# Performance work log

Measured on AMD Instinct MI355X. Metric: run time of the kernel, lower is better.

## Reference

```python
import jax, jax.numpy as jnp
import numpy as np

D_MODEL = 1024
N_HEADS = 16
B, T = 2, 2048


def setup_inputs() -> dict:
    key = jax.random.key(0)
    kx, kqkv, ko = jax.random.split(key, 3)
    x = jax.random.normal(kx, (B, T, D_MODEL), dtype=jnp.float32)
    # flax Linear default init (lecun_normal ~ scaled); plain scaled normal is fine for a baseline
    Wqkv = jax.random.normal(kqkv, (D_MODEL, 3 * D_MODEL), dtype=jnp.float32) / np.sqrt(D_MODEL)
    Wo = jax.random.normal(ko, (D_MODEL, D_MODEL), dtype=jnp.float32) / np.sqrt(D_MODEL)
    return {"x": x, "Wqkv": Wqkv, "Wo": Wo}


def reference(x, Wqkv, Wo):
    Bx, Tx, C = x.shape
    H = N_HEADS
    Hd = C // H
    scale = C ** (-0.5)  # NOTE: module scales by d_model**-0.5, not head_dim**-0.5
    qkv = x @ Wqkv  # [B, T, 3C]
    q, k, v = jnp.split(qkv, 3, axis=-1)
    q = q.reshape(Bx, Tx, H, Hd).transpose(0, 2, 1, 3)  # [B,H,T,Hd]
    k = k.reshape(Bx, Tx, H, Hd).transpose(0, 2, 1, 3)
    v = v.reshape(Bx, Tx, H, Hd).transpose(0, 2, 1, 3)
    attn = jnp.einsum('bhid,bhjd->bhij', q, k) * scale  # [B,H,T,T]
    mask = jnp.tril(jnp.ones((Tx, Tx), dtype=jnp.bool_))
    attn = jnp.where(mask[None, None], attn, jnp.finfo(attn.dtype).min)
    attn = jax.nn.softmax(attn.astype(jnp.float32), axis=-1).astype(attn.dtype)
    out = jnp.einsum('bhij,bhjd->bhid', attn, v)  # [B,H,T,Hd]
    out = out.transpose(0, 2, 1, 3).reshape(Bx, Tx, C)
    return out @ Wo
```

## Files before the change

kernel.cpp:

```cpp
#include <hip/hip_runtime.h>
#include <cstdint>
#include <math.h>

#define D_MODEL 1024
#define N_HEADS 16
#define HEAD_DIM 64
#define BB 2
#define TT 2048
#define QSCALE 0.04508422002778011f
#define MSTATIC 12.0f

typedef float f32x4 __attribute__((ext_vector_type(4)));
typedef __bf16 bf16x8 __attribute__((ext_vector_type(8)));

__device__ inline ushort f2bf(float f) {
    union { float f; uint32_t u; } c; c.f = f;
    uint32_t u = c.u;
    uint32_t r = (u + 0x7FFFu + ((u >> 16) & 1u)) >> 16;
    return (ushort)r;
}
__device__ inline ushort f2bf_hw(float f) {
    __bf16 h = (__bf16)f;
    return __builtin_bit_cast(ushort, h);
}

__device__ inline void load_lds16(const ushort* g, ushort* lds_uniform_base) {
    __builtin_amdgcn_global_load_lds(
        (const __attribute__((address_space(1))) uint32_t*)g,
        (__attribute__((address_space(3))) uint32_t*)lds_uniform_base, 16, 0, 0);
}

__global__ __launch_bounds__(256) void prep(
    const float4* __restrict__ xin, ushort4* __restrict__ xb,
    const float* __restrict__ Wqkv, ushort* __restrict__ WqkvT,
    const float* __restrict__ Wo, ushort* __restrict__ WoT)
{
    int bid = blockIdx.x;
    int tid = threadIdx.x;
    if (bid < 4096) {
        int i = bid * 256 + tid;
        float4 v = xin[i];
        ushort4 u;
        u.x = f2bf(v.x); u.y = f2bf(v.y); u.z = f2bf(v.z); u.w = f2bf(v.w);
        xb[i] = u;
        return;
    }
    __shared__ ushort tile[32][33];
    int tx = tid & 31, ty = tid >> 5;
    const float* in; ushort* out; int R, C, c0, r0;
    if (bid < 7168) {
        int b2 = bid - 4096;
        in = Wqkv; out = WqkvT; R = D_MODEL; C = 3 * D_MODEL;
        c0 = (b2 % 96) * 32; r0 = (b2 / 96) * 32;
    } else {
        int b3 = bid - 7168;
        in = Wo; out = WoT; R = D_MODEL; C = D_MODEL;
        c0 = (b3 % 32) * 32; r0 = (b3 / 32) * 32;
    }
#pragma unroll
    for (int i = 0; i < 32; i += 8)
        tile[ty + i][tx] = f2bf(in[(size_t)(r0 + ty + i) * C + (c0 + tx)]);
    __syncthreads();
#pragma unroll
    for (int i = 0; i < 32; i += 8)
        out[(size_t)(c0 + ty + i) * R + (r0 + tx)] = tile[tx][ty + i];
}

__global__ __launch_bounds__(256) void transpose_v_bf16(
    const ushort* __restrict__ in, ushort* __restrict__ out)
{
    int z = blockIdx.z;
    const ushort* ip = in + (size_t)z * TT * HEAD_DIM;
    ushort* op = out + (size_t)z * TT * HEAD_DIM;
    __shared__ ushort tile[32][33];
    int tx = threadIdx.x, ty = threadIdx.y;
    int d0 = blockIdx.x * 32;
    int t0 = blockIdx.y * 32;
#pragma unroll
    for (int i = 0; i < 32; i += 8)
        tile[ty + i][tx] = ip[(size_t)(t0 + ty + i) * HEAD_DIM + d0 + tx];
    __syncthreads();
#pragma unroll
    for (int i = 0; i < 32; i += 8)
        op[(size_t)(d0 + ty + i) * TT + t0 + tx] = tile[tx][ty + i];
}

__device__ inline void gemm128_mainloop(
    const ushort* __restrict__ A, const ushort* __restrict__ BT,
    int rowBase, int colBase, ushort* Al, ushort* Bl,
    f32x4 acc[4][4], int wave, int lane)
{
    const int K = D_MODEL;
    int lr = lane & 15, quad = lane >> 4;
    int lrow = lane >> 2;
    int kq = lane & 3;
    int mq = (wave >> 1) * 64, nq = (wave & 1) * 64;

    const ushort* gA0 = A + (size_t)(rowBase + wave * 32 + lrow) * K + kq * 8;
    const ushort* gA1 = gA0 + (size_t)16 * K;
    const ushort* gB0 = BT + (size_t)(colBase + wave * 32 + lrow) * K + kq * 8;
    const ushort* gB1 = gB0 + (size_t)16 * K;
    ushort* lA0 = Al + (wave * 32) * 32;
    ushort* lA1 = Al + (wave * 32 + 16) * 32;
    ushort* lB0 = Bl + (wave * 32) * 32;
    ushort* lB1 = Bl + (wave * 32 + 16) * 32;

    for (int kt = 0; kt < K / 32; ++kt) {
        __syncthreads();
        int ko = kt * 32;
        load_lds16(gA0 + ko, lA0);
        load_lds16(gA1 + ko, lA1);
        load_lds16(gB0 + ko, lB0);
        load_lds16(gB1 + ko, lB1);
        __syncthreads();
        bf16x8 af[4], bf[4];
#pragma unroll
        for (int mi = 0; mi < 4; ++mi)
            af[mi] = *(const bf16x8*)(Al + (mq + mi * 16 + lr) * 32 + quad * 8);
#pragma unroll
        for (int ni = 0; ni < 4; ++ni)
            bf[ni] = *(const bf16x8*)(Bl + (nq + ni * 16 + lr) * 32 + quad * 8);
#pragma unroll
        for (int mi = 0; mi < 4; ++mi)
#pragma unroll
            for (int ni = 0; ni < 4; ++ni)
                acc[mi][ni] = __builtin_amdgcn_mfma_f32_16x16x32_bf16(
                    af[mi], bf[ni], acc[mi][ni], 0, 0, 0);
    }
}

__global__ __launch_bounds__(256) void gemm_qkv(
    const ushort* __restrict__ A, const ushort* __restrict__ BT,
    ushort* __restrict__ Qo, ushort* __restrict__ Ko, ushort* __restrict__ Vo)
{
    __shared__ ushort Al[128 * 32];
    __shared__ ushort Bl[128 * 32];
    int tid = threadIdx.x;
    int wave = tid >> 6, lane = tid & 63;
    int lr = lane & 15, quad = lane >> 4;
    int rowBase = blockIdx.y * 128;
    int colBase = blockIdx.x * 128;
    f32x4 acc[4][4] = {};
    gemm128_mainloop(A, BT, rowBase, colBase, Al, Bl, acc, wave, lane);

    int mq = (wave >> 1) * 64, nq = (wave & 1) * 64;
#pragma unroll
    for (int ni = 0; ni < 4; ++ni) {
        int n = colBase + nq + ni * 16 + lr;
        int s = n >> 10;
        int cc = n & 1023;
        int h = cc >> 6, d = cc & 63;
        ushort* dst = (s == 0) ? Qo : (s == 1 ? Ko : Vo);
        float scale = (s == 0) ? QSCALE : 1.0f;
#pragma unroll
        for (int mi = 0; mi < 4; ++mi) {
#pragma unroll
            for (int i = 0; i < 4; ++i) {
                int m = rowBase + mq + mi * 16 + quad * 4 + i;
                int b = m >> 11, t = m & 2047;
                int bh = b * N_HEADS + h;
                dst[((size_t)bh * TT + t) * HEAD_DIM + d] = f2bf(acc[mi][ni][i] * scale);
            }
        }
    }
}

__global__ __launch_bounds__(256) void gemm_plain(
    const ushort* __restrict__ A, const ushort* __restrict__ BT,
    float* __restrict__ O, int N)
{
    const int K = D_MODEL;
    __shared__ ushort Al[128 * 32];
    __shared__ ushort Bl[64 * 32];
    int tid = threadIdx.x;
    int wave = tid >> 6, lane = tid & 63;
    int lr = lane & 15, quad = lane >> 4;
    int lrow = lane >> 2, kq = lane & 3;
    int rowBase = blockIdx.y * 128;
    int colBase = blockIdx.x * 64;
    int mq = (wave >> 1) * 64, nq = (wave & 1) * 32;

    const ushort* gA0 = A + (size_t)(rowBase + wave * 32 + lrow) * K + kq * 8;
    const ushort* gA1 = gA0 + (size_t)16 * K;
    const ushort* gB0 = BT + (size_t)(colBase + wave * 32 + lrow) * K + kq * 8;
    const ushort* gB1 = gB0 + (size_t)16 * K;
    ushort* lA0 = Al + (wave * 32) * 32;
    ushort* lA1 = Al + (wave * 32 + 16) * 32;
    ushort* lB0 = Bl + (wave * 32) * 32;
    ushort* lB1 = Bl + (wave * 32 + 16) * 32;

    f32x4 acc[4][2] = {};
    for (int kt = 0; kt < K / 32; ++kt) {
        __syncthreads();
        int ko = kt * 32;
        load_lds16(gA0 + ko, lA0);
        load_lds16(gA1 + ko, lA1);
        if (wave < 2) {
            load_lds16(gB0 + ko, lB0);
            load_lds16(gB1 + ko, lB1);
        }
        __syncthreads();
        bf16x8 af[4], bf[2];
#pragma unroll
        for (int mi = 0; mi < 4; ++mi)
            af[mi] = *(const bf16x8*)(Al + (mq + mi * 16 + lr) * 32 + quad * 8);
#pragma unroll
        for (int ni = 0; ni < 2; ++ni)
            bf[ni] = *(const bf16x8*)(Bl + (nq + ni * 16 + lr) * 32 + quad * 8);
#pragma unroll
        for (int mi = 0; mi < 4; ++mi)
#pragma unroll
            for (int ni = 0; ni < 2; ++ni)
                acc[mi][ni] = __builtin_amdgcn_mfma_f32_16x16x32_bf16(
                    af[mi], bf[ni], acc[mi][ni], 0, 0, 0);
    }

#pragma unroll
    for (int mi = 0; mi < 4; ++mi)
#pragma unroll
        for (int ni = 0; ni < 2; ++ni) {
            int n = colBase + nq + ni * 16 + lr;
#pragma unroll
            for (int i = 0; i < 4; ++i) {
                int m = rowBase + mq + mi * 16 + quad * 4 + i;
                O[(size_t)m * N + n] = acc[mi][ni][i];
            }
        }
}

__global__ __launch_bounds__(256) void attn_flash(
    const ushort* __restrict__ Q,
    const ushort* __restrict__ K,
    const ushort* __restrict__ VT,
    ushort* __restrict__ AO)
{
    int bid = blockIdx.x;
    int bh  = bid >> 4;
    int idx = bid & 15;
    int tid = threadIdx.x;
    int wave = tid >> 6, lane = tid & 63;
    int quad = lane >> 4, lr = lane & 15;

    int a    = idx * 4 + wave;
    int Gl   = a;
    int Gh   = 127 - a;
    int rowl = Gl << 4;
    int rowh = Gh << 4;
    int liml = Gl >> 1;
    int limh = Gh >> 1;
    int bt64 = 32 - idx;

    const ushort* Qb = Q  + (size_t)bh * TT * HEAD_DIM;
    const ushort* Kb = K  + (size_t)bh * TT * HEAD_DIM;
    const ushort* Vb = VT + (size_t)bh * HEAD_DIM * TT;

    __shared__ ushort Kl[2][8 * 64 * 8];
    __shared__ ushort Vl[2][8 * 64 * 8];
    __shared__ ushort pbuf[4][32][40];
    ushort (*P)[40] = pbuf[wave];

    const ushort* gK0 = Kb + (size_t)lane * HEAD_DIM + wave * 8;
    const ushort* gK1 = Kb + (size_t)lane * HEAD_DIM + (wave + 4) * 8;
    const ushort* gV0 = Vb + (size_t)lane * TT + wave * 8;
    const ushort* gV1 = Vb + (size_t)lane * TT + 32 + wave * 8;

    bf16x8 qa[2][2];
#pragma unroll
    for (int r = 0; r < 2; ++r) {
        int rb = (r == 0) ? rowl : rowh;
#pragma unroll
        for (int s = 0; s < 2; ++s)
            qa[r][s] = *(const bf16x8*)(Qb + (size_t)(rb + lr) * HEAD_DIM
                                           + s * 32 + quad * 8);
    }

    f32x4 o[2][4] = {};
    f32x4 l[2] = {};

    bf16x8 ones;
#pragma unroll
    for (int j = 0; j < 8; ++j) ones[j] = (__bf16)1.0f;

    load_lds16(gK0, Kl[0] + wave * 512);
    load_lds16(gK1, Kl[0] + (wave + 4) * 512);
    load_lds16(gV0, Vl[0] + wave * 512);
    load_lds16(gV1, Vl[0] + (wave + 4) * 512);
    __syncthreads();

    for (int kt64 = 0; kt64 < bt64; ++kt64) {
        int cur = kt64 & 1;
        if (kt64 + 1 < bt64) {
            size_t koff = (size_t)(kt64 + 1) * 64;
            ushort* KlN = Kl[cur ^ 1];
            ushort* VlN = Vl[cur ^ 1];
            load_lds16(gK0 + koff * HEAD_DIM, KlN + wave * 512);
            load_lds16(gK1 + koff * HEAD_DIM, KlN + (wave + 4) * 512);
            load_lds16(gV0 + koff, VlN + wave * 512);
            load_lds16(gV1 + koff, VlN + (wave + 4) * 512);
        }
        const ushort* Klc = Kl[cur];
        const ushort* Vlc = Vl[cur];

#pragma unroll
        for (int sub = 0; sub < 2; ++sub) {
            int kt32 = kt64 * 2 + sub;
            if (kt32 > limh) break;
            int act0 = (kt32 <= liml);

            bf16x8 kb[2][2];
#pragma unroll
            for (int c = 0; c < 2; ++c)
#pragma unroll
                for (int s = 0; s < 2; ++s)
                    kb[c][s] = *(const bf16x8*)&Klc[(((s * 4 + quad) * 64)
                                 + sub * 32 + c * 16 + lr) * 8];
            bf16x8 vb[4];
#pragma unroll
            for (int d = 0; d < 4; ++d)
                vb[d] = *(const bf16x8*)&Vlc[(((sub * 4 + quad) * 64)
                             + d * 16 + lr) * 8];

#pragma unroll
            for (int r = 0; r < 2; ++r) {
                if (r == 0 && !act0) continue;
                int rb  = (r == 0) ? rowl : rowh;
                int lim = (r == 0) ? liml : limh;

                f32x4 sc[2];
#pragma unroll
                for (int c = 0; c < 2; ++c)
#pragma unroll
                    for (int i = 0; i < 4; ++i) sc[c][i] = -MSTATIC;
#pragma unroll
                for (int c = 0; c < 2; ++c) {
                    sc[c] = __builtin_amdgcn_mfma_f32_16x16x32_bf16(qa[r][0], kb[c][0], sc[c], 0, 0, 0);
                    sc[c] = __builtin_amdgcn_mfma_f32_16x16x32_bf16(qa[r][1], kb[c][1], sc[c], 0, 0, 0);
                }
                if (kt32 == lim) {
#pragma unroll
                    for (int c = 0; c < 2; ++c)
#pragma unroll
                        for (int i = 0; i < 4; ++i)
                            if (kt32 * 32 + c * 16 + lr > rb + quad * 4 + i)
                                sc[c][i] = -3e38f;
                }
#pragma unroll
                for (int c = 0; c < 2; ++c)
#pragma unroll
                    for (int i = 0; i < 4; ++i)
                        P[r * 16 + quad * 4 + i][c * 16 + lr] =
                            f2bf_hw(__builtin_amdgcn_exp2f(sc[c][i]));
            }

#pragma unroll
            for (int r = 0; r < 2; ++r) {
                if (r == 0 && !act0) continue;
                bf16x8 pa = *(const bf16x8*)&P[r * 16 + lr][quad * 8];
                l[r] = __builtin_amdgcn_mfma_f32_16x16x32_bf16(pa, ones, l[r], 0, 0, 0);
#pragma unroll
                for (int d = 0; d < 4; ++d)
                    o[r][d] = __builtin_amdgcn_mfma_f32_16x16x32_bf16(pa, vb[d], o[r][d], 0, 0, 0);
            }
        }
        __syncthreads();
    }

    int b = bh >> 4, h = bh & 15;
#pragma unroll
    for (int r = 0; r < 2; ++r) {
        int rb = (r == 0) ? rowl : rowh;
        f32x4 rl;
#pragma unroll
        for (int i = 0; i < 4; ++i) rl[i] = 1.0f / l[r][i];
#pragma unroll
        for (int d = 0; d < 4; ++d)
#pragma unroll
            for (int i = 0; i < 4; ++i) {
                int row = rb + quad * 4 + i;
                AO[((size_t)(b * TT + row)) * D_MODEL + h * HEAD_DIM + d * 16 + lr] =
                    f2bf(o[r][d][i] * rl[i]);
            }
    }
}

extern "C" void kernel_launch(void* const* d_in, const int* in_sizes, int n_in,
                              void* d_out, int out_size, void* d_ws, size_t ws_size,
                              hipStream_t stream)
{
    (void)in_sizes; (void)n_in; (void)out_size; (void)ws_size;
    const float* x    = (const float*)d_in[0];
    const float* Wqkv = (const float*)d_in[1];
    const float* Wo   = (const float*)d_in[2];
    float* out = (float*)d_out;

    char* ws = (char*)d_ws;
    size_t off = 0;
    ushort* WqkvT = (ushort*)(ws + off); off += (size_t)3 * D_MODEL * D_MODEL * 2;
    ushort* WoT   = (ushort*)(ws + off); off += (size_t)D_MODEL * D_MODEL * 2;
    ushort* xb    = (ushort*)(ws + off); off += (size_t)BB * TT * D_MODEL * 2;
    ushort* Qd    = (ushort*)(ws + off); off += (size_t)BB * D_MODEL * TT * 2;
    ushort* Kd    = (ushort*)(ws + off); off += (size_t)BB * D_MODEL * TT * 2;
    ushort* Vd    = (ushort*)(ws + off); off += (size_t)BB * D_MODEL * TT * 2;
    ushort* VTd   = (ushort*)(ws + off); off += (size_t)BB * D_MODEL * TT * 2;
    ushort* AO    = (ushort*)(ws + off); off += (size_t)BB * TT * D_MODEL * 2;

    prep<<<dim3(8192), 256, 0, stream>>>(
        (const float4*)x, (ushort4*)xb, Wqkv, WqkvT, Wo, WoT);

    gemm_qkv<<<dim3(3 * D_MODEL / 128, BB * TT / 128), 256, 0, stream>>>(
        xb, WqkvT, Qd, Kd, Vd);

    transpose_v_bf16<<<dim3(HEAD_DIM / 32, TT / 32, BB * N_HEADS), dim3(32, 8), 0, stream>>>(
        Vd, VTd);

    attn_flash<<<dim3(512), 256, 0, stream>>>(Qd, Kd, VTd, AO);

    gemm_plain<<<dim3(D_MODEL / 64, BB * TT / 128), 256, 0, stream>>>(
        AO, WoT, out, D_MODEL);
}
```

Baseline: 196.1 us.

## Rewrite attention with 32x32 MFMA tiles and register-resident P via permlane swap

The flash attention kernel moves from 16x16x32 to 32x32x16 MFMA tiles. It computes S transposed (K as A operand) so the exponentiated probabilities can be repacked into the PV operand with v_permlane32_swap instead of a round trip through LDS. Row sums come from a scalar add plus a permlane swap rather than an extra MFMA against a ones vector. Blocks shrink to 2 waves with 32-row query groups, and block ids are remapped so each XCD handles the same heads for better L2 locality. The trade-off is higher register pressure and fewer waves per block, which may reduce latency hiding.

```diff
diff --git a/kernel.cpp b/kernel.cpp
--- a/kernel.cpp
+++ b/kernel.cpp
@@ -11,7 +11,9 @@
 #define MSTATIC 12.0f
 
 typedef float f32x4 __attribute__((ext_vector_type(4)));
+typedef float f32x16 __attribute__((ext_vector_type(16)));
 typedef __bf16 bf16x8 __attribute__((ext_vector_type(8)));
+typedef unsigned int u32x4 __attribute__((ext_vector_type(4)));
 
 __device__ inline ushort f2bf(float f) {
     union { float f; uint32_t u; } c; c.f = f;
@@ -22,6 +24,9 @@
 __device__ inline ushort f2bf_hw(float f) {
     __bf16 h = (__bf16)f;
     return __builtin_bit_cast(ushort, h);
+}
+__device__ inline void pl32swap(unsigned int& x, unsigned int& y) {
+    asm volatile("v_permlane32_swap_b32 %0, %1" : "+v"(x), "+v"(y));
 }
 
 __device__ inline void load_lds16(const ushort* g, ushort* lds_uniform_base) {
@@ -228,27 +233,26 @@
         }
 }
 
-__global__ __launch_bounds__(256) void attn_flash(
+__global__ __launch_bounds__(128, 1) void attn_flash(
     const ushort* __restrict__ Q,
     const ushort* __restrict__ K,
     const ushort* __restrict__ VT,
     ushort* __restrict__ AO)
 {
     int bid = blockIdx.x;
-    int bh  = bid >> 4;
-    int idx = bid & 15;
+    int xcd = bid & 7;
+    int sl  = bid >> 3;
+    int bh  = (sl >> 4) * 8 + xcd;
+    int u   = sl & 15;
     int tid = threadIdx.x;
-    int wave = tid >> 6, lane = tid & 63;
-    int quad = lane >> 4, lr = lane & 15;
-
-    int a    = idx * 4 + wave;
-    int Gl   = a;
-    int Gh   = 127 - a;
-    int rowl = Gl << 4;
-    int rowh = Gh << 4;
-    int liml = Gl >> 1;
-    int limh = Gh >> 1;
-    int bt64 = 32 - idx;
+    int w    = tid >> 6;
+    int lane = tid & 63;
+    int l31 = lane & 31, hi = lane >> 5;
+
+    int a  = u * 2 + w;
+    int gs = a;
+    int gd = 63 - a;
+    int bt64 = 32 - u;
 
     const ushort* Qb = Q  + (size_t)bh * TT * HEAD_DIM;
     const ushort* Kb = K  + (size_t)bh * TT * HEAD_DIM;
@@ -256,47 +260,49 @@
 
     __shared__ ushort Kl[2][8 * 64 * 8];
     __shared__ ushort Vl[2][8 * 64 * 8];
-    __shared__ ushort pbuf[4][32][40];
-    ushort (*P)[40] = pbuf[wave];
-
-    const ushort* gK0 = Kb + (size_t)lane * HEAD_DIM + wave * 8;
-    const ushort* gK1 = Kb + (size_t)lane * HEAD_DIM + (wave + 4) * 8;
-    const ushort* gV0 = Vb + (size_t)lane * TT + wave * 8;
-    const ushort* gV1 = Vb + (size_t)lane * TT + 32 + wave * 8;
-
-    bf16x8 qa[2][2];
-#pragma unroll
-    for (int r = 0; r < 2; ++r) {
-        int rb = (r == 0) ? rowl : rowh;
-#pragma unroll
-        for (int s = 0; s < 2; ++s)
-            qa[r][s] = *(const bf16x8*)(Qb + (size_t)(rb + lr) * HEAD_DIM
-                                           + s * 32 + quad * 8);
-    }
-
-    f32x4 o[2][4] = {};
-    f32x4 l[2] = {};
-
-    bf16x8 ones;
-#pragma unroll
-    for (int j = 0; j < 8; ++j) ones[j] = (__bf16)1.0f;
-
-    load_lds16(gK0, Kl[0] + wave * 512);
-    load_lds16(gK1, Kl[0] + (wave + 4) * 512);
-    load_lds16(gV0, Vl[0] + wave * 512);
-    load_lds16(gV1, Vl[0] + (wave + 4) * 512);
+
+    const ushort* gK[4];
+    const ushort* gV[4];
+#pragma unroll
+    for (int t = 0; t < 4; ++t) {
+        gK[t] = Kb + (size_t)lane * HEAD_DIM + (w * 4 + t) * 8;
+        gV[t] = Vb + (size_t)lane * TT + (w * 4 + t) * 8;
+    }
+
+    int rb[2] = { gs << 5, gd << 5 };
+    bf16x8 qa[2][4];
+#pragma unroll
+    for (int gi = 0; gi < 2; ++gi)
+#pragma unroll
+        for (int si = 0; si < 4; ++si)
+            qa[gi][si] = *(const bf16x8*)(Qb + (size_t)(rb[gi] + l31) * HEAD_DIM
+                                             + si * 16 + hi * 8);
+
+    f32x16 o[2][2];
+#pragma unroll
+    for (int gi = 0; gi < 2; ++gi)
+#pragma unroll
+        for (int dh = 0; dh < 2; ++dh)
+#pragma unroll
+            for (int i = 0; i < 16; ++i) o[gi][dh][i] = 0.0f;
+    float l[2] = { 0.0f, 0.0f };
+
+#pragma unroll
+    for (int t = 0; t < 4; ++t) {
+        load_lds16(gK[t], Kl[0] + (w * 4 + t) * 512);
+        load_lds16(gV[t], Vl[0] + (w * 4 + t) * 512);
+    }
     __syncthreads();
 
     for (int kt64 = 0; kt64 < bt64; ++kt64) {
         int cur = kt64 & 1;
         if (kt64 + 1 < bt64) {
             size_t koff = (size_t)(kt64 + 1) * 64;
-            ushort* KlN = Kl[cur ^ 1];
-            ushort* VlN = Vl[cur ^ 1];
-            load_lds16(gK0 + koff * HEAD_DIM, KlN + wave * 512);
-            load_lds16(gK1 + koff * HEAD_DIM, KlN + (wave + 4) * 512);
-            load_lds16(gV0 + koff, VlN + wave * 512);
-            load_lds16(gV1 + koff, VlN + (wave + 4) * 512);
+#pragma unroll
+            for (int t = 0; t < 4; ++t) {
+                load_lds16(gK[t] + koff * HEAD_DIM, Kl[cur ^ 1] + (w * 4 + t) * 512);
+                load_lds16(gV[t] + koff,            Vl[cur ^ 1] + (w * 4 + t) * 512);
+            }
         }
         const ushort* Klc = Kl[cur];
         const ushort* Vlc = Vl[cur];
@@ -304,81 +310,113 @@
 #pragma unroll
         for (int sub = 0; sub < 2; ++sub) {
             int kt32 = kt64 * 2 + sub;
-            if (kt32 > limh) break;
-            int act0 = (kt32 <= liml);
-
-            bf16x8 kb[2][2];
-#pragma unroll
-            for (int c = 0; c < 2; ++c)
-#pragma unroll
-                for (int s = 0; s < 2; ++s)
-                    kb[c][s] = *(const bf16x8*)&Klc[(((s * 4 + quad) * 64)
-                                 + sub * 32 + c * 16 + lr) * 8];
-            bf16x8 vb[4];
-#pragma unroll
-            for (int d = 0; d < 4; ++d)
-                vb[d] = *(const bf16x8*)&Vlc[(((sub * 4 + quad) * 64)
-                             + d * 16 + lr) * 8];
-
-#pragma unroll
-            for (int r = 0; r < 2; ++r) {
-                if (r == 0 && !act0) continue;
-                int rb  = (r == 0) ? rowl : rowh;
-                int lim = (r == 0) ? liml : limh;
-
-                f32x4 sc[2];
-#pragma unroll
-                for (int c = 0; c < 2; ++c)
-#pragma unroll
-                    for (int i = 0; i < 4; ++i) sc[c][i] = -MSTATIC;
-#pragma unroll
-                for (int c = 0; c < 2; ++c) {
-                    sc[c] = __builtin_amdgcn_mfma_f32_16x16x32_bf16(qa[r][0], kb[c][0], sc[c], 0, 0, 0);
-                    sc[c] = __builtin_amdgcn_mfma_f32_16x16x32_bf16(qa[r][1], kb[c][1], sc[c], 0, 0, 0);
+            if (kt32 > gd) break;
+
+            bf16x8 kb[4];
+#pragma unroll
+            for (int si = 0; si < 4; ++si)
+                kb[si] = *(const bf16x8*)&Klc[((si * 2 + hi) * 64 + sub * 32 + l31) * 8];
+            bf16x8 vb[2][2];
+#pragma unroll
+            for (int kh = 0; kh < 2; ++kh)
+#pragma unroll
+                for (int dh = 0; dh < 2; ++dh)
+                    vb[kh][dh] = *(const bf16x8*)&Vlc[((sub * 4 + kh * 2 + hi) * 64
+                                     + dh * 32 + l31) * 8];
+
+#pragma unroll
+            for (int gi = 0; gi < 2; ++gi) {
+                int g = (gi == 0) ? gs : gd;
+                if (gi == 0 && kt32 > gs) continue;
+
+                f32x16 sc;
+#pragma unroll
+                for (int i = 0; i < 16; ++i) sc[i] = -MSTATIC;
+#pragma unroll
+                for (int si = 0; si < 4; ++si)
+                    sc = __builtin_amdgcn_mfma_f32_32x32x16_bf16(
+                        kb[si], qa[gi][si], sc, 0, 0, 0);
+
+                if (kt32 == g) {
+#pragma unroll
+                    for (int r = 0; r < 16; ++r) {
+                        int krow = (r & 3) + 8 * (r >> 2) + 4 * hi;
+                        if (krow > l31) sc[r] = -3e38f;
+                    }
                 }
-                if (kt32 == lim) {
-#pragma unroll
-                    for (int c = 0; c < 2; ++c)
-#pragma unroll
-                        for (int i = 0; i < 4; ++i)
-                            if (kt32 * 32 + c * 16 + lr > rb + quad * 4 + i)
-                                sc[c][i] = -3e38f;
+
+                ushort bb[16];
+#pragma unroll
+                for (int r = 0; r < 16; ++r)
+                    bb[r] = f2bf_hw(__builtin_amdgcn_exp2f(sc[r]));
+
+                float pb[16];
+#pragma unroll
+                for (int r = 0; r < 16; ++r)
+                    pb[r] = __builtin_bit_cast(float, (unsigned int)bb[r] << 16);
+                float rs = (((pb[0] + pb[1]) + (pb[2] + pb[3]))
+                          + ((pb[4] + pb[5]) + (pb[6] + pb[7])))
+                         + (((pb[8] + pb[9]) + (pb[10] + pb[11]))
+                          + ((pb[12] + pb[13]) + (pb[14] + pb[15])));
+                unsigned int xu = __builtin_bit_cast(unsigned int, rs);
+                unsigned int yu = xu;
+                pl32swap(xu, yu);
+                l[gi] += __builtin_bit_cast(float, xu)
+                       + __builtin_bit_cast(float, yu);
+
+                unsigned int C0 = (unsigned int)bb[0]  | ((unsigned int)bb[1]  << 16);
+                unsigned int C1 = (unsigned int)bb[2]  | ((unsigned int)bb[3]  << 16);
+                unsigned int C2 = (unsigned int)bb[4]  | ((unsigned int)bb[5]  << 16);
+                unsigned int C3 = (unsigned int)bb[6]  | ((unsigned int)bb[7]  << 16);
+                unsigned int C4 = (unsigned int)bb[8]  | ((unsigned int)bb[9]  << 16);
+                unsigned int C5 = (unsigned int)bb[10] | ((unsigned int)bb[11] << 16);
+                unsigned int C6 = (unsigned int)bb[12] | ((unsigned int)bb[13] << 16);
+                unsigned int C7 = (unsigned int)bb[14] | ((unsigned int)bb[15] << 16);
+                unsigned int d00 = C0, d02 = C2; pl32swap(d00, d02);
+                unsigned int d01 = C1, d03 = C3; pl32swap(d01, d03);
+                unsigned int d10 = C4, d12 = C6; pl32swap(d10, d12);
+                unsigned int d11 = C5, d13 = C7; pl32swap(d11, d13);
+                u32x4 w0; w0.x = d00; w0.y = d01; w0.z = d02; w0.w = d03;
+                u32x4 w1; w1.x = d10; w1.y = d11; w1.z = d12; w1.w = d13;
+                bf16x8 pa0 = __builtin_bit_cast(bf16x8, w0);
+                bf16x8 pa1 = __builtin_bit_cast(bf16x8, w1);
+
+#pragma unroll
+                for (int dh = 0; dh < 2; ++dh) {
+                    o[gi][dh] = __builtin_amdgcn_mfma_f32_32x32x16_bf16(
+                        pa0, vb[0][dh], o[gi][dh], 0, 0, 0);
+                    o[gi][dh] = __builtin_amdgcn_mfma_f32_32x32x16_bf16(
+                        pa1, vb[1][dh], o[gi][dh], 0, 0, 0);
                 }
-#pragma unroll
-                for (int c = 0; c < 2; ++c)
-#pragma unroll
-                    for (int i = 0; i < 4; ++i)
-                        P[r * 16 + quad * 4 + i][c * 16 + lr] =
-                            f2bf_hw(__builtin_amdgcn_exp2f(sc[c][i]));
             }
-
-#pragma unroll
-            for (int r = 0; r < 2; ++r) {
-                if (r == 0 && !act0) continue;
-                bf16x8 pa = *(const bf16x8*)&P[r * 16 + lr][quad * 8];
-                l[r] = __builtin_amdgcn_mfma_f32_16x16x32_bf16(pa, ones, l[r], 0, 0, 0);
-#pragma unroll
-                for (int d = 0; d < 4; ++d)
-                    o[r][d] = __builtin_amdgcn_mfma_f32_16x16x32_bf16(pa, vb[d], o[r][d], 0, 0, 0);
-            }
         }
         __syncthreads();
     }
 
+    float* lf = (float*)&Kl[0][0];
+    if (hi == 0) {
+        lf[(w * 2 + 0) * 32 + l31] = l[0];
+        lf[(w * 2 + 1) * 32 + l31] = l[1];
+    }
+    __syncthreads();
+
     int b = bh >> 4, h = bh & 15;
 #pragma unroll
-    for (int r = 0; r < 2; ++r) {
-        int rb = (r == 0) ? rowl : rowh;
-        f32x4 rl;
-#pragma unroll
-        for (int i = 0; i < 4; ++i) rl[i] = 1.0f / l[r][i];
-#pragma unroll
-        for (int d = 0; d < 4; ++d)
-#pragma unroll
-            for (int i = 0; i < 4; ++i) {
-                int row = rb + quad * 4 + i;
-                AO[((size_t)(b * TT + row)) * D_MODEL + h * HEAD_DIM + d * 16 + lr] =
-                    f2bf(o[r][d][i] * rl[i]);
+    for (int gi = 0; gi < 2; ++gi) {
+        f32x4 rl[4];
+#pragma unroll
+        for (int r4 = 0; r4 < 4; ++r4) {
+            f32x4 lv = *(const f32x4*)&lf[(w * 2 + gi) * 32 + r4 * 8 + hi * 4];
+#pragma unroll
+            for (int i = 0; i < 4; ++i) rl[r4][i] = 1.0f / lv[i];
+        }
+#pragma unroll
+        for (int dh = 0; dh < 2; ++dh)
+#pragma unroll
+            for (int r = 0; r < 16; ++r) {
+                int row = rb[gi] + (r & 3) + 8 * (r >> 2) + 4 * hi;
+                AO[((size_t)(b * TT + row)) * D_MODEL + h * HEAD_DIM + dh * 32 + l31] =
+                    f2bf(o[gi][dh][r] * rl[r >> 2][r & 3]);
             }
     }
 }
@@ -413,7 +451,7 @@
     transpose_v_bf16<<<dim3(HEAD_DIM / 32, TT / 32, BB * N_HEADS), dim3(32, 8), 0, stream>>>(
         Vd, VTd);
 
-    attn_flash<<<dim3(512), 256, 0, stream>>>(Qd, Kd, VTd, AO);
+    attn_flash<<<dim3(512), 128, 0, stream>>>(Qd, Kd, VTd, AO);
 
     gemm_plain<<<dim3(D_MODEL / 64, BB * TT / 128), 256, 0, stream>>>(
         AO, WoT, out, D_MODEL);
```

Result: slower. 212.0 us (+8.1%).
